# Performance work log

Measured on AMD Instinct MI355X. Metric: run time of the kernel, lower is better.

## Reference

```python
import jax, jax.numpy as jnp
import numpy as np

N_NODES = 4096
HID = 64
N_STEP = 10
_OFFSETS = np.array([1, 2, 5, 11, 23, 47, 97, 193])  # circulant graph -> degree 16


def setup_inputs() -> dict:
    rng = np.random.default_rng(0)
    N = N_NODES
    i = np.repeat(np.arange(N), len(_OFFSETS))
    j = (i + np.tile(_OFFSETS, N)) % N
    vals = rng.normal(0.0, 0.5, i.shape).astype(np.float32)
    J = np.zeros((N, N), np.float32)
    J[i, j] = vals
    J[j, i] = vals  # symmetric coupling matrix
    row, col = np.nonzero(J)                      # E directed edges, row-major sorted
    key_fwd = row.astype(np.int64) * N + col
    rev = np.searchsorted(key_fwd, col.astype(np.int64) * N + row)  # reverse-edge index
    ru, cu = np.nonzero(np.triu(J))               # Eu upper-triangular edges
    u2e = np.searchsorted(key_fwd, ru.astype(np.int64) * N + cu)    # upper -> full edge index
    bias = rng.normal(0.0, 0.5, N).astype(np.float32)
    p = lambda *s: jnp.asarray(rng.normal(0.0, 0.1, s).astype(np.float32))
    return {
        'J': jnp.asarray(J), 'bias': jnp.asarray(bias),
        'gat_W': p(4, HID), 'gat_a': p(2 * HID, 1),
        'ci_W1': p(4, HID), 'ci_b1': jnp.zeros((HID,), jnp.float32),
        'ci_W2': p(HID, HID), 'ci_b2': jnp.zeros((HID,), jnp.float32),
        'ci_W3': p(HID, 1), 'ci_b3': jnp.zeros((1,), jnp.float32),
        'row': jnp.asarray(row.astype(np.int32)), 'col': jnp.asarray(col.astype(np.int32)),
        'rev': jnp.asarray(rev.astype(np.int32)),
        'ru': jnp.asarray(ru.astype(np.int32)), 'cu': jnp.asarray(cu.astype(np.int32)),
        'u2e': jnp.asarray(u2e.astype(np.int32)),
        'N_step': N_STEP, 'MPNNtype': 0,
    }


def reference(J, bias, gat_W, gat_a, ci_W1, ci_b1, ci_W2, ci_b2, ci_W3, ci_b3,
              row, col, rev, ru, cu, u2e, N_step, MPNNtype):
    N = J.shape[0]
    adj = (jnp.abs(J) > 0).astype(J.dtype)
    # node features: [-b, b, degree, row-sum of J]
    feat = jnp.stack([-bias, bias, adj.sum(1), J.sum(1)], axis=1)  # [N,4]
    # GAT scores: e[i,j] = leakyrelu([Wh_i || Wh_j] @ a) = leakyrelu(Wh_i@a1 + Wh_j@a2)
    Wh = feat @ gat_W                                  # [N,H]
    f1 = Wh @ gat_a[:HID, 0]
    f2 = Wh @ gat_a[HID:, 0]
    e = jax.nn.leaky_relu(f1[:, None] + f2[None, :], 0.2)
    att = jnp.where(adj > 0, jnp.exp(e), 0.0)
    Cij_matrix = 0.5 * (att + att.T)                   # [N,N]
    Cij_e = Cij_matrix[row, col]                       # [E]
    # Ci readout MLP
    h = jax.nn.relu(feat @ ci_W1 + ci_b1)
    h = jax.nn.relu(h @ ci_W2 + ci_b2)
    Ci = h @ ci_W3 + ci_b3                             # [N,1]
    dom = Ci + Cij_matrix.sum(1, keepdims=True)
    dom = jnp.sign(dom) * jnp.maximum(jnp.abs(dom), 0.1)  # clamp |.| >= 0.1
    bias_scale = bias / dom[:, 0]
    bx_scale = jnp.stack([-bias_scale, bias_scale], axis=1)  # [N,2]
    Jv = J[row, col]
    Jxy_scale = jnp.stack([jnp.stack([Jv, -Jv], -1),
                           jnp.stack([-Jv, Jv], -1)], axis=1) / Cij_e[:, None, None]  # [E,2,2]

    def node_update(em):
        # node_messages[j,:] = sum over edges (i->j) of em[e,:]
        nm = jax.ops.segment_sum(em, col, num_segments=N) / dom   # [N,2]
        lnZ = jnp.log(jnp.sum(jnp.exp(bx_scale + nm), axis=1, keepdims=True))
        return bx_scale + nm - lnZ, lnZ

    em0 = jnp.zeros((row.shape[0], 2), J.dtype)  # log of all-ones messages
    hidden0, lnZ0 = node_update(em0)

    def bp_step(carry, _):
        em, hidden, lnZ = carry
        ln_pj = hidden[row][:, :, None]     # [E,2,1]
        ln_zj = lnZ[row][:, :, None]        # [E,1,1]
        ln_mu_ij = em[rev][:, :, None]      # message on reverse edge, [E,2,1]
        M = jnp.exp(Jxy_scale + ln_pj + ln_zj - ln_mu_ij)          # [E,2,2]
        M = M / jnp.sum(jnp.max(M, axis=1), axis=1)[:, None, None]
        em_new = jnp.log(jnp.max(M ** Cij_e[:, None, None], axis=1))  # [E,2]
        hidden_new, lnZ_new = node_update(em_new)
        return (em_new, hidden_new, lnZ_new), None

    (em, hidden, lnZ), _ = jax.lax.scan(bp_step, (em0, hidden0, lnZ0), None, length=N_step)

    readout = jnp.exp(hidden)                           # [N,2]
    Js = J[ru, cu] / Cij_matrix[ru, cu]                 # [Eu]
    Jxy_u = jnp.exp(jnp.stack([jnp.stack([Js, -Js], -1),
                               jnp.stack([-Js, Js], -1)], axis=1))  # [Eu,2,2]
    temp_i = readout[cu] / jnp.exp(em[u2e])             # [Eu,2]
    temp_j = readout[ru] / jnp.exp(em[rev[u2e]])        # [Eu,2]
    pw = Jxy_u * temp_i[:, None, :] * temp_j[:, :, None]
    pw = pw / jnp.sum(pw, axis=(1, 2), keepdims=True)
    readout_pairwise = pw.reshape(-1, 4)                # [Eu,4]
    Cij_u = Cij_matrix[ru, cu]
    node_H = -jnp.sum(readout * jnp.log(readout + 1e-16), axis=1)
    edge_H = -jnp.sum(readout_pairwise * jnp.log(readout_pairwise + 1e-16), axis=1)
    node_entropy = Ci[:, 0] @ jax.lax.stop_gradient(node_H)
    edge_entropy = Cij_u @ jax.lax.stop_gradient(edge_H)
    return (readout, readout_pairwise, node_entropy + edge_entropy,
            node_entropy, edge_entropy, Ci[:, 0], Cij_u, dom)
```

## Files before the change

### kernel.cpp

```cpp
#include <hip/hip_runtime.h>
#include <cstddef>

#define TB    512
#define NB    128
#define NSTEP 10
#define SENTV 0xFFFFFFFFFFFFFFFFULL

__device__ __forceinline__ float lse2(float a, float b) {
    return fmaxf(a, b) + __logf(1.0f + __expf(-fabsf(a - b)));
}

__device__ __forceinline__ void stA(float2* p, float2 v) {
    union { float2 f; unsigned long long u; } x; x.f = v;
    __hip_atomic_store((unsigned long long*)p, x.u,
                       __ATOMIC_RELAXED, __HIP_MEMORY_SCOPE_AGENT);
}
__device__ __forceinline__ float2 pollLd(const float2* p) {
    union { float2 f; unsigned long long u; } x;
    x.u = __hip_atomic_load((const unsigned long long*)p,
                            __ATOMIC_RELAXED, __HIP_MEMORY_SCOPE_AGENT);
    while (x.u == SENTV) {
        __builtin_amdgcn_s_sleep(1);
        x.u = __hip_atomic_load((const unsigned long long*)p,
                                __ATOMIC_RELAXED, __HIP_MEMORY_SCOPE_AGENT);
    }
    return x.f;
}

struct KParams {
    const float *J, *bias, *gat_W, *gat_a, *W1, *b1, *W2, *b2, *W3, *b3;
    const int *col, *rev, *ru, *cu, *u2e;
    int N, Eu;
    float2 *fA, *jsC, *em, *uS;
    float  *ci_out, *dom_out, *ent;
    float2* ro_out;
    float4* rp_out;
    float*  cij_out;
};

__global__ __launch_bounds__(TB) void k_fused(KParams p) {
    __shared__ float4 sW2T[64 * 17];
    __shared__ float  sh1[TB / 16][68];
    __shared__ float  red[TB / 64];

    const int tidb = threadIdx.x;
    const int g = blockIdx.x * TB + tidb;
    const int i = g >> 4, t = g & 15;
    const int lane = tidb & 63;
    const int N = p.N;

    for (int idx = tidb; idx < 64 * 16; idx += TB) {
        const int o = idx >> 4, hh = idx & 15;
        sW2T[o * 17 + hh] = make_float4(
            p.W2[(4 * hh + 0) * 64 + o], p.W2[(4 * hh + 1) * 64 + o],
            p.W2[(4 * hh + 2) * 64 + o], p.W2[(4 * hh + 3) * 64 + o]);
    }
    if (g < 3) {
        __hip_atomic_store((int*)&p.ent[g], 0,
                           __ATOMIC_RELAXED, __HIP_MEMORY_SCOPE_AGENT);
    }

    const int j  = p.col[g];
    const float Jv = p.J[(size_t)i * (size_t)N + (size_t)j];

    float rs = Jv;
    rs += __shfl_xor(rs, 1); rs += __shfl_xor(rs, 2);
    rs += __shfl_xor(rs, 4); rs += __shfl_xor(rs, 8);

    const float bi = p.bias[i];

    float s8 = 0.0f;
    if (lane < 8) {
        int k = lane & 3;
        const float* a = p.gat_a + ((lane < 4) ? 0 : 64);
        for (int h = 0; h < 64; ++h) s8 += p.gat_W[k * 64 + h] * a[h];
    }
    const float w10 = __shfl(s8, 0), w11 = __shfl(s8, 1), w12 = __shfl(s8, 2), w13 = __shfl(s8, 3);
    const float w20 = __shfl(s8, 4), w21 = __shfl(s8, 5), w22 = __shfl(s8, 6), w23 = __shfl(s8, 7);
    const float fd = 16.0f;
    const float f1i = -bi * w10 + bi * w11 + fd * w12 + rs * w13;
    const float f2i = -bi * w20 + bi * w21 + fd * w22 + rs * w23;
    if (t == 0) stA(&p.fA[i], make_float2(f1i, f2i));

    const int nib = tidb >> 4;
    #pragma unroll
    for (int m = 0; m < 4; ++m) {
        int h = t + 16 * m;
        float a = -bi * p.W1[h] + bi * p.W1[64 + h] + fd * p.W1[128 + h]
                + rs * p.W1[192 + h] + p.b1[h];
        sh1[nib][h] = fmaxf(a, 0.0f);
    }
    __syncthreads();
    float4 hv[16];
    {
        const float4* hrow = (const float4*)&sh1[nib][0];
        #pragma unroll
        for (int hh = 0; hh < 16; ++hh) hv[hh] = hrow[hh];
    }
    float civ = 0.0f;
    #pragma unroll
    for (int m = 0; m < 4; ++m) {
        const int o = t + 16 * m;
        const float4* wrow = &sW2T[o * 17];
        float acc = p.b2[o];
        #pragma unroll
        for (int hh = 0; hh < 16; ++hh) {
            const float4 wv = wrow[hh];
            acc += hv[hh].x * wv.x + hv[hh].y * wv.y
                 + hv[hh].z * wv.z + hv[hh].w * wv.w;
        }
        civ += fmaxf(acc, 0.0f) * p.W3[o];
    }
    civ += __shfl_xor(civ, 1); civ += __shfl_xor(civ, 2);
    civ += __shfl_xor(civ, 4); civ += __shfl_xor(civ, 8);
    const float ci = civ + p.b3[0];

    const float2 fj = pollLd(&p.fA[j]);
    float x1 = f1i + fj.y; x1 = (x1 > 0.0f) ? x1 : 0.2f * x1;
    float x2 = fj.x + f2i; x2 = (x2 > 0.0f) ? x2 : 0.2f * x2;
    const float C  = 0.5f * (__expf(x1) + __expf(x2));
    const float js = Jv / C;
    stA(&p.jsC[g], make_float2(js, C));

    float sc = C;
    sc += __shfl_xor(sc, 1); sc += __shfl_xor(sc, 2);
    sc += __shfl_xor(sc, 4); sc += __shfl_xor(sc, 8);
    const float s  = ci + sc;
    const float cl = fmaxf(fabsf(s), 0.1f);
    const float d  = (s > 0.0f) ? cl : ((s < 0.0f) ? -cl : 0.0f);
    const float rd = 1.0f / d;
    const float bs = bi * rd;
    if (t == 0) {
        p.ci_out[i] = ci;
        p.dom_out[i] = d;
        stA(&p.uS[i], make_float2(-bs, bs));
    }

    int eE = 0, eR = 0, eC = 0, eEr = 0;
    if (g < p.Eu) {
        eE = p.u2e[g]; eR = p.ru[g]; eC = p.cu[g];
        eEr = p.rev[eE];
    }

    float in0 = 0.0f, in1 = 0.0f;
    float out0 = 0.0f, out1 = 0.0f;
    float ui0 = -bs, ui1 = bs;
    for (int st = 0; st < NSTEP; ++st) {
        const float2 uj = pollLd(&p.uS[(size_t)st * N + j]);
        const float a0 = uj.x - out0, a1 = uj.y - out1;
        const float t0 = fmaxf( js + a0, -js + a1);
        const float t1 = fmaxf(-js + a0,  js + a1);
        const float ls = lse2(t0, t1);
        const float ni0 = C * (t0 - ls), ni1 = C * (t1 - ls);
        const float pu0 = ui0, pu1 = ui1;
        const float pi0 = in0, pi1 = in1;
        in0 = ni0; in1 = ni1;

        float nm0 = in0, nm1 = in1;
        nm0 += __shfl_xor(nm0, 1); nm1 += __shfl_xor(nm1, 1);
        nm0 += __shfl_xor(nm0, 2); nm1 += __shfl_xor(nm1, 2);
        nm0 += __shfl_xor(nm0, 4); nm1 += __shfl_xor(nm1, 4);
        nm0 += __shfl_xor(nm0, 8); nm1 += __shfl_xor(nm1, 8);
        ui0 = -bs + nm0 * rd; ui1 = bs + nm1 * rd;
        if (t == 0) stA(&p.uS[(size_t)(st + 1) * N + i], make_float2(ui0, ui1));
        if (st == NSTEP - 1) stA(&p.em[g], make_float2(in0, in1));

        const float b0 = pu0 - pi0, b1 = pu1 - pi1;
        const float q0 = fmaxf( js + b0, -js + b1);
        const float q1 = fmaxf(-js + b0,  js + b1);
        const float qs = lse2(q0, q1);
        out0 = C * (q0 - qs); out1 = C * (q1 - qs);
    }

    float nodeC = 0.0f;
    if (t == 0) {
        const float lz = lse2(ui0, ui1);
        const float r0 = __expf(ui0 - lz), r1 = __expf(ui1 - lz);
        p.ro_out[i] = make_float2(r0, r1);
        const float H = -(r0 * __logf(r0 + 1e-16f) + r1 * __logf(r1 + 1e-16f));
        nodeC = ci * H;
    }
    for (int off = 32; off > 0; off >>= 1) nodeC += __shfl_down(nodeC, off);
    {
        const int wv = tidb >> 6;
        if (lane == 0) red[wv] = nodeC;
        __syncthreads();
        if (tidb == 0) {
            float sn = 0.0f;
            #pragma unroll
            for (int w = 0; w < TB / 64; ++w) sn += red[w];
            atomicAdd(&p.ent[0], sn);
            atomicAdd(&p.ent[1], sn);
        }
        __syncthreads();
    }

    const float2* uF = p.uS + (size_t)NSTEP * N;
    float edgeC = 0.0f;
    if (g < p.Eu) {
        const float2 jc = pollLd(&p.jsC[eE]);
        const float jse = jc.x, Ce = jc.y;
        const float2 uc = pollLd(&uF[eC]), ur = pollLd(&uF[eR]);
        const float2 eme = pollLd(&p.em[eEr]);
        const float2 emr = pollLd(&p.em[eE]);
        const float lc = lse2(uc.x, uc.y);
        const float lr = lse2(ur.x, ur.y);
        const float ti0 = (uc.x - lc) - eme.x, ti1 = (uc.y - lc) - eme.y;
        const float tj0 = (ur.x - lr) - emr.x, tj1 = (ur.y - lr) - emr.y;
        const float L00 =  jse + ti0 + tj0;
        const float L01 = -jse + ti1 + tj0;
        const float L10 = -jse + ti0 + tj1;
        const float L11 =  jse + ti1 + tj1;
        const float mL = fmaxf(fmaxf(L00, L01), fmaxf(L10, L11));
        float p00 = __expf(L00 - mL), p01 = __expf(L01 - mL);
        float p10 = __expf(L10 - mL), p11 = __expf(L11 - mL);
        const float inv = 1.0f / (p00 + p01 + p10 + p11);
        p00 *= inv; p01 *= inv; p10 *= inv; p11 *= inv;
        p.rp_out[g] = make_float4(p00, p01, p10, p11);
        p.cij_out[g] = Ce;
        const float H = -(p00 * __logf(p00 + 1e-16f) + p01 * __logf(p01 + 1e-16f)
                        + p10 * __logf(p10 + 1e-16f) + p11 * __logf(p11 + 1e-16f));
        edgeC = Ce * H;
    }
    for (int off = 32; off > 0; off >>= 1) edgeC += __shfl_down(edgeC, off);
    const int wv = tidb >> 6;
    if (lane == 0) red[wv] = edgeC;
    __syncthreads();
    if (tidb == 0) {
        float se = 0.0f;
        #pragma unroll
        for (int w = 0; w < TB / 64; ++w) se += red[w];
        atomicAdd(&p.ent[0], se);
        atomicAdd(&p.ent[2], se);
    }
}

extern "C" void kernel_launch(void* const* d_in, const int* in_sizes, int n_in,
                              void* d_out, int out_size, void* d_ws, size_t ws_size,
                              hipStream_t stream) {
    const int N  = in_sizes[1];
    const int E  = in_sizes[10];
    const int Eu = in_sizes[13];

    float* out = (float*)d_out;
    size_t OFF_RP  = 2 * (size_t)N;
    size_t OFF_ENT = OFF_RP + 4 * (size_t)Eu;

    char* w = (char*)d_ws;
    auto carve = [&](size_t bytes) {
        void* q = (void*)w;
        w += (bytes + 255) & ~(size_t)255;
        return q;
    };

    KParams p;
    p.J     = (const float*)d_in[0];
    p.bias  = (const float*)d_in[1];
    p.gat_W = (const float*)d_in[2];
    p.gat_a = (const float*)d_in[3];
    p.W1    = (const float*)d_in[4];
    p.b1    = (const float*)d_in[5];
    p.W2    = (const float*)d_in[6];
    p.b2    = (const float*)d_in[7];
    p.W3    = (const float*)d_in[8];
    p.b3    = (const float*)d_in[9];
    p.col   = (const int*)d_in[11];
    p.rev   = (const int*)d_in[12];
    p.ru    = (const int*)d_in[13];
    p.cu    = (const int*)d_in[14];
    p.u2e   = (const int*)d_in[15];
    p.N = N; p.Eu = Eu;

    const size_t szFA = (size_t)N * 8;
    const size_t szJC = (size_t)E * 8;
    const size_t szEM = (size_t)E * 8;
    const size_t szUS = (size_t)(NSTEP + 1) * N * 8;
    p.fA  = (float2*)carve(szFA);
    p.jsC = (float2*)carve(szJC);
    p.em  = (float2*)carve(szEM);
    p.uS  = (float2*)carve(szUS);

    p.ro_out  = (float2*)out;
    p.rp_out  = (float4*)(out + OFF_RP);
    p.ent     = out + OFF_ENT;
    p.ci_out  = p.ent + 3;
    p.cij_out = p.ci_out + N;
    p.dom_out = p.cij_out + Eu;

    hipMemsetAsync(p.fA, 0xFF, szFA + szJC + szEM + szUS, stream);
    k_fused<<<dim3(NB), dim3(TB), 0, stream>>>(p);
}
```

Before: 157.3 us.

## Push node messages to per-edge mailboxes instead of gathering by neighbor index

Each edge thread now writes its node's values into the reverse edge's slot, so the consumer polls its own contiguous slot instead of gathering scattered node entries. This applies to the GAT features, the initial message and every BP step's node message. The GAT weight-by-attention dot products are also spread across the whole wavefront with a shuffle reduction instead of an 8-lane serial loop. In exchange there are 16x more atomic stores, scattered to rev indices, and a larger scratch buffer (NSTEP*E float2) that must be memset to the sentinel each call.

Result: no change. 157.1 us (-0.1%).

```diff
diff --git a/kernel.cpp b/kernel.cpp
--- a/kernel.cpp
+++ b/kernel.cpp
@@ -31,7 +31,7 @@
     const float *J, *bias, *gat_W, *gat_a, *W1, *b1, *W2, *b2, *W3, *b3;
     const int *col, *rev, *ru, *cu, *u2e;
     int N, Eu;
-    float2 *fA, *jsC, *em, *uS;
+    float2 *fAIn, *jsC, *em, *uIn, *uFin;
     float  *ci_out, *dom_out, *ent;
     float2* ro_out;
     float4* rp_out;
@@ -47,7 +47,7 @@
     const int g = blockIdx.x * TB + tidb;
     const int i = g >> 4, t = g & 15;
     const int lane = tidb & 63;
-    const int N = p.N;
+    const int E = p.N * 16;
 
     for (int idx = tidb; idx < 64 * 16; idx += TB) {
         const int o = idx >> 4, hh = idx & 15;
@@ -61,7 +61,8 @@
     }
 
     const int j  = p.col[g];
-    const float Jv = p.J[(size_t)i * (size_t)N + (size_t)j];
+    const int rg = p.rev[g];
+    const float Jv = p.J[(size_t)i * (size_t)p.N + (size_t)j];
 
     float rs = Jv;
     rs += __shfl_xor(rs, 1); rs += __shfl_xor(rs, 2);
@@ -70,17 +71,23 @@
     const float bi = p.bias[i];
 
     float s8 = 0.0f;
-    if (lane < 8) {
-        int k = lane & 3;
-        const float* a = p.gat_a + ((lane < 4) ? 0 : 64);
-        for (int h = 0; h < 64; ++h) s8 += p.gat_W[k * 64 + h] * a[h];
-    }
-    const float w10 = __shfl(s8, 0), w11 = __shfl(s8, 1), w12 = __shfl(s8, 2), w13 = __shfl(s8, 3);
-    const float w20 = __shfl(s8, 4), w21 = __shfl(s8, 5), w22 = __shfl(s8, 6), w23 = __shfl(s8, 7);
+    {
+        const int d8 = lane >> 3, c8 = lane & 7;
+        const int kk = d8 & 3;
+        const float* ga = p.gat_a + ((d8 < 4) ? 0 : 64);
+        #pragma unroll
+        for (int h = 0; h < 8; ++h)
+            s8 += p.gat_W[kk * 64 + 8 * c8 + h] * ga[8 * c8 + h];
+        s8 += __shfl_xor(s8, 1); s8 += __shfl_xor(s8, 2); s8 += __shfl_xor(s8, 4);
+    }
+    const float w10 = __shfl(s8, 0),  w11 = __shfl(s8, 8);
+    const float w12 = __shfl(s8, 16), w13 = __shfl(s8, 24);
+    const float w20 = __shfl(s8, 32), w21 = __shfl(s8, 40);
+    const float w22 = __shfl(s8, 48), w23 = __shfl(s8, 56);
     const float fd = 16.0f;
     const float f1i = -bi * w10 + bi * w11 + fd * w12 + rs * w13;
     const float f2i = -bi * w20 + bi * w21 + fd * w22 + rs * w23;
-    if (t == 0) stA(&p.fA[i], make_float2(f1i, f2i));
+    stA(&p.fAIn[rg], make_float2(f1i, f2i));
 
     const int nib = tidb >> 4;
     #pragma unroll
@@ -115,7 +122,7 @@
     civ += __shfl_xor(civ, 4); civ += __shfl_xor(civ, 8);
     const float ci = civ + p.b3[0];
 
-    const float2 fj = pollLd(&p.fA[j]);
+    const float2 fj = pollLd(&p.fAIn[g]);
     float x1 = f1i + fj.y; x1 = (x1 > 0.0f) ? x1 : 0.2f * x1;
     float x2 = fj.x + f2i; x2 = (x2 > 0.0f) ? x2 : 0.2f * x2;
     const float C  = 0.5f * (__expf(x1) + __expf(x2));
@@ -133,8 +140,8 @@
     if (t == 0) {
         p.ci_out[i] = ci;
         p.dom_out[i] = d;
-        stA(&p.uS[i], make_float2(-bs, bs));
-    }
+    }
+    stA(&p.uIn[rg], make_float2(-bs, bs));
 
     int eE = 0, eR = 0, eC = 0, eEr = 0;
     if (g < p.Eu) {
@@ -146,7 +153,7 @@
     float out0 = 0.0f, out1 = 0.0f;
     float ui0 = -bs, ui1 = bs;
     for (int st = 0; st < NSTEP; ++st) {
-        const float2 uj = pollLd(&p.uS[(size_t)st * N + j]);
+        const float2 uj = pollLd(&p.uIn[(size_t)st * E + g]);
         const float a0 = uj.x - out0, a1 = uj.y - out1;
         const float t0 = fmaxf( js + a0, -js + a1);
         const float t1 = fmaxf(-js + a0,  js + a1);
@@ -162,8 +169,12 @@
         nm0 += __shfl_xor(nm0, 4); nm1 += __shfl_xor(nm1, 4);
         nm0 += __shfl_xor(nm0, 8); nm1 += __shfl_xor(nm1, 8);
         ui0 = -bs + nm0 * rd; ui1 = bs + nm1 * rd;
-        if (t == 0) stA(&p.uS[(size_t)(st + 1) * N + i], make_float2(ui0, ui1));
-        if (st == NSTEP - 1) stA(&p.em[g], make_float2(in0, in1));
+        if (st < NSTEP - 1) {
+            stA(&p.uIn[(size_t)(st + 1) * E + rg], make_float2(ui0, ui1));
+        } else {
+            if (t == 0) stA(&p.uFin[i], make_float2(ui0, ui1));
+            stA(&p.em[g], make_float2(in0, in1));
+        }
 
         const float b0 = pu0 - pi0, b1 = pu1 - pi1;
         const float q0 = fmaxf( js + b0, -js + b1);
@@ -195,12 +206,11 @@
         __syncthreads();
     }
 
-    const float2* uF = p.uS + (size_t)NSTEP * N;
     float edgeC = 0.0f;
     if (g < p.Eu) {
         const float2 jc = pollLd(&p.jsC[eE]);
         const float jse = jc.x, Ce = jc.y;
-        const float2 uc = pollLd(&uF[eC]), ur = pollLd(&uF[eR]);
+        const float2 uc = pollLd(&p.uFin[eC]), ur = pollLd(&p.uFin[eR]);
         const float2 eme = pollLd(&p.em[eEr]);
         const float2 emr = pollLd(&p.em[eE]);
         const float lc = lse2(uc.x, uc.y);
@@ -271,14 +281,16 @@
     p.u2e   = (const int*)d_in[15];
     p.N = N; p.Eu = Eu;
 
-    const size_t szFA = (size_t)N * 8;
+    const size_t szFA = (size_t)E * 8;
     const size_t szJC = (size_t)E * 8;
     const size_t szEM = (size_t)E * 8;
-    const size_t szUS = (size_t)(NSTEP + 1) * N * 8;
-    p.fA  = (float2*)carve(szFA);
-    p.jsC = (float2*)carve(szJC);
-    p.em  = (float2*)carve(szEM);
-    p.uS  = (float2*)carve(szUS);
+    const size_t szUI = (size_t)NSTEP * E * 8;
+    const size_t szUF = (size_t)N * 8;
+    p.fAIn = (float2*)carve(szFA);
+    p.jsC  = (float2*)carve(szJC);
+    p.em   = (float2*)carve(szEM);
+    p.uIn  = (float2*)carve(szUI);
+    p.uFin = (float2*)carve(szUF);
 
     p.ro_out  = (float2*)out;
     p.rp_out  = (float4*)(out + OFF_RP);
@@ -287,6 +299,6 @@
     p.cij_out = p.ci_out + N;
     p.dom_out = p.cij_out + Eu;
 
-    hipMemsetAsync(p.fA, 0xFF, szFA + szJC + szEM + szUS, stream);
+    hipMemsetAsync(p.fAIn, 0xFF, szFA + szJC + szEM + szUI + szUF, stream);
     k_fused<<<dim3(NB), dim3(TB), 0, stream>>>(p);
 }
```
